# Optimization experiments

Measured on AMD Instinct MI355X. Metric: run time of the kernel, lower is better.

## Reference

```python
import jax, jax.numpy as jnp
import numpy as np

N = 16384          # number of units
K = 655
BOOST_STRENGTH = 1.0


def setup_inputs() -> dict:
    key = jax.random.key(0)
    k1, k2 = jax.random.split(key)
    x = jax.random.normal(k1, (4096, N), dtype=jnp.float32)
    dutyCycle = jax.random.uniform(k2, (N,), dtype=jnp.float32)
    return {"x": x, "dutyCycle": dutyCycle}


def reference(x, dutyCycle):
    # boost factor per unit: encourages under-used units
    targetDensity = K / x.shape[1]
    boostFactors = jnp.exp((targetDensity - dutyCycle) * BOOST_STRENGTH)  # (N,)
    boosted = x * boostFactors  # (B, N)
    # top-k per row, then scatter a binary mask of winners
    _, idx = jax.lax.top_k(boosted, K)  # (B, K)
    b = jnp.arange(x.shape[0])[:, None]  # (B, 1)
    res = jnp.zeros_like(x).at[b, idx].set(1.0)
    return res
```

## Files before the change

### kernel.cpp

```cpp
#include <hip/hip_runtime.h>
#include <math.h>
#include <stdint.h>


#define N_UNITS 16384
#define K_WIN 655
#define NT 512
#define NPROBE 11
#define SCAP 256
#define ITERS (N_UNITS / (NT * 4))

__device__ __forceinline__ uint32_t fkey(float f) {
    uint32_t b = __float_as_uint(f);
    uint32_t m = (uint32_t)((int32_t)b >> 31) | 0x80000000u;
    return b ^ m;
}

__global__ void boost_kernel(const float* __restrict__ duty,
                             float* __restrict__ bf, int n) {
    int i = blockIdx.x * blockDim.x + threadIdx.x;
    if (i < n) {
        const float td = 0.03997802734375f;
        float s = td - duty[i];
        bf[i] = (float)exp((double)s);
    }
}

__global__ __launch_bounds__(NT, 1) void kwinners_kernel(
    const float* __restrict__ x, const float* __restrict__ bf,
    float* __restrict__ out) {
    __shared__ uint32_t red[(NT / 64) * NPROBE];
    __shared__ int cglob[NPROBE];
    __shared__ uint32_t s_key[SCAP];
    __shared__ uint32_t s_idx[SCAP];
    __shared__ uint32_t bmap[N_UNITS / 32];
    __shared__ int sc[1];

    const int tid = threadIdx.x;
    const int lane = tid & 63;
    const int w = tid >> 6;
    const int row = blockIdx.x;
    const float4* xrow = (const float4*)(x + (size_t)row * N_UNITS);
    const float4* bfv = (const float4*)bf;
    float* orow = out + (size_t)row * N_UNITS;

    bmap[tid] = 0u;
    if (tid == 0) sc[0] = 0;

    uint32_t PF[NPROBE];
    {
        const float pv[NPROBE] = {1.90f, 1.70f, 1.55f, 1.43f, 1.33f, 1.25f,
                                  1.18f, 1.12f, 1.06f, 0.99f, 0.90f};
#pragma unroll
        for (int p = 0; p < NPROBE; ++p) PF[p] = fkey(pv[p]) | 0xFFFFu;
    }

    int cnt[NPROBE];
#pragma unroll
    for (int p = 0; p < NPROBE; ++p) cnt[p] = 0;

    uint4 kk[ITERS];

#pragma unroll
    for (int j = 0; j < ITERS; ++j) {
        int i4 = tid + j * NT;
        float4 xv = xrow[i4];
        float4 bv = bfv[i4];
        kk[j].x = fkey(xv.x * bv.x);
        kk[j].y = fkey(xv.y * bv.y);
        kk[j].z = fkey(xv.z * bv.z);
        kk[j].w = fkey(xv.w * bv.w);
#pragma unroll
        for (int p = 0; p < NPROBE; ++p)
            cnt[p] += (kk[j].x > PF[p]) + (kk[j].y > PF[p]) +
                      (kk[j].z > PF[p]) + (kk[j].w > PF[p]);
    }

    auto reduce_counts = [&]() {
#pragma unroll
        for (int p = 0; p < NPROBE; ++p) {
            int v = cnt[p];
#pragma unroll
            for (int m2 = 32; m2 >= 1; m2 >>= 1) v += __shfl_xor(v, m2, 64);
            if (lane == 0) red[w * NPROBE + p] = (uint32_t)v;
        }
        __syncthreads();
        if (tid < NPROBE) {
            int s = 0;
#pragma unroll
            for (int ww = 0; ww < NT / 64; ++ww) s += (int)red[ww * NPROBE + tid];
            cglob[tid] = s;
        }
        __syncthreads();
    };
    reduce_counts();

    long lo, hi;
    int cab, cgl;
    {
        int j = 0;
        while (j < NPROBE && cglob[j] < K_WIN) ++j;
        if (j == 0) {
            lo = (long)PF[0]; cgl = cglob[0]; hi = 0xFFFFFFFFL; cab = 0;
        } else if (j == NPROBE) {
            lo = -1; cgl = N_UNITS; hi = (long)PF[NPROBE - 1];
            cab = cglob[NPROBE - 1];
        } else {
            lo = (long)PF[j]; cgl = cglob[j]; hi = (long)PF[j - 1];
            cab = cglob[j - 1];
        }
    }
    int inB = cgl - cab;

    while (inB > SCAP && (hi - lo) > 1) {
        unsigned long range = (unsigned long)(hi - lo);
#pragma unroll
        for (int p = 0; p < NPROBE; ++p) {
            long Tp = lo + (long)(range * (unsigned long)(NPROBE - p) /
                                  (NPROBE + 1));
            int c = 0;
#pragma unroll
            for (int j = 0; j < ITERS; ++j)
                c += ((long)kk[j].x > Tp) + ((long)kk[j].y > Tp) +
                     ((long)kk[j].z > Tp) + ((long)kk[j].w > Tp);
            cnt[p] = c;
        }
        reduce_counts();
        int j = 0;
        while (j < NPROBE && cglob[j] < K_WIN) ++j;
        const long llo = lo;
        auto Tof = [&](int p) {
            return llo + (long)(range * (unsigned long)(NPROBE - p) /
                                (NPROBE + 1));
        };
        if (j == 0) {
            lo = Tof(0); cgl = cglob[0];
        } else if (j == NPROBE) {
            hi = Tof(NPROBE - 1); cab = cglob[NPROBE - 1];
        } else {
            lo = Tof(j); cgl = cglob[j]; hi = Tof(j - 1); cab = cglob[j - 1];
        }
        inB = cgl - cab;
    }
    const int need = K_WIN - cab;

    if (inB <= SCAP) {
#pragma unroll
        for (int j = 0; j < ITERS; ++j) {
            int base = (tid + j * NT) * 4;
            uint32_t kv[4] = {kk[j].x, kk[j].y, kk[j].z, kk[j].w};
#pragma unroll
            for (int e = 0; e < 4; ++e) {
                long k = (long)kv[e];
                if (k > lo && k <= hi) {
                    int p = atomicAdd(&sc[0], 1);
                    if (p < SCAP) {
                        s_key[p] = kv[e];
                        s_idx[p] = (uint32_t)(base + e);
                    }
                }
            }
        }
        __syncthreads();
        const int sS = sc[0];

        for (int jj = tid; jj < sS; jj += NT) {
            uint32_t myk = s_key[jj];
            uint32_t myi = s_idx[jj];
            int r = 0;
            for (int l = 0; l < sS; ++l) {
                uint32_t lk = s_key[l];
                r += (lk > myk) || (lk == myk && s_idx[l] < myi);
            }
            if (r < need) atomicOr(&bmap[myi >> 5], 1u << (myi & 31));
        }
    } else {
        if (tid == 0) {
            const float* xr = x + (size_t)row * N_UNITS;
            int r = 0;
            for (int i = 0; i < N_UNITS && r < need; ++i) {
                uint32_t kf = fkey(xr[i] * bf[i]);
                if ((long)kf == hi) {
                    bmap[i >> 5] |= (1u << (i & 31));
                    ++r;
                }
            }
        }
    }
    __syncthreads();

#pragma unroll
    for (int j = 0; j < ITERS; ++j) {
        int f = tid + j * NT;
        uint32_t bm = bmap[f >> 3];
        int sh = (f & 7) * 4;
        float4 o;
        o.x = (((long)kk[j].x > hi) || ((bm >> (sh + 0)) & 1u)) ? 1.0f : 0.0f;
        o.y = (((long)kk[j].y > hi) || ((bm >> (sh + 1)) & 1u)) ? 1.0f : 0.0f;
        o.z = (((long)kk[j].z > hi) || ((bm >> (sh + 2)) & 1u)) ? 1.0f : 0.0f;
        o.w = (((long)kk[j].w > hi) || ((bm >> (sh + 3)) & 1u)) ? 1.0f : 0.0f;
        ((float4*)orow)[f] = o;
    }
}

extern "C" void kernel_launch(void* const* d_in, const int* in_sizes, int n_in,
                              void* d_out, int out_size, void* d_ws,
                              size_t ws_size, hipStream_t stream) {
    const float* x = (const float*)d_in[0];
    const float* duty = (const float*)d_in[1];
    float* out = (float*)d_out;
    float* bf = (float*)d_ws;

    hipLaunchKernelGGL(boost_kernel, dim3(N_UNITS / 256), dim3(256), 0, stream,
                       duty, bf, N_UNITS);
    int rows = out_size / N_UNITS;
    hipLaunchKernelGGL(kwinners_kernel, dim3(rows), dim3(NT), 0, stream, x, bf,
                       out);
}
```

Baseline: 516.4 us.

## Prefetch row loads upfront, retune probe thresholds, pack keys for ranking

All x and boost-factor float4 loads for a row are issued before any key computation. This puts every load in flight at once and hides global-memory latency. The first-pass probe set drops from 11 to 7 thresholds concentrated near the expected cutoff, and the candidate buffer grows from 256 to 320, so fewer rows should need refinement passes. Candidate key and index are packed into one 64-bit value so ranking is a single compare, and the long compares become 32-bit compares. The cost is higher register pressure from holding the whole row twice.

New measurement: 439.0 us. 15.0% less time.

```diff
diff --git a/kernel.cpp b/kernel.cpp
--- a/kernel.cpp
+++ b/kernel.cpp
@@ -6,8 +6,8 @@
 #define N_UNITS 16384
 #define K_WIN 655
 #define NT 512
-#define NPROBE 11
-#define SCAP 256
+#define NPROBE 7
+#define SCAP 320
 #define ITERS (N_UNITS / (NT * 4))
 
 __device__ __forceinline__ uint32_t fkey(float f) {
@@ -31,8 +31,7 @@
     float* __restrict__ out) {
     __shared__ uint32_t red[(NT / 64) * NPROBE];
     __shared__ int cglob[NPROBE];
-    __shared__ uint32_t s_key[SCAP];
-    __shared__ uint32_t s_idx[SCAP];
+    __shared__ unsigned long long s_pk[SCAP];
     __shared__ uint32_t bmap[N_UNITS / 32];
     __shared__ int sc[1];
 
@@ -49,27 +48,30 @@
 
     uint32_t PF[NPROBE];
     {
-        const float pv[NPROBE] = {1.90f, 1.70f, 1.55f, 1.43f, 1.33f, 1.25f,
-                                  1.18f, 1.12f, 1.06f, 0.99f, 0.90f};
+        const float pv[NPROBE] = {1.45f, 1.32f, 1.24f, 1.20f,
+                                  1.16f, 1.10f, 1.00f};
 #pragma unroll
         for (int p = 0; p < NPROBE; ++p) PF[p] = fkey(pv[p]) | 0xFFFFu;
     }
 
+    float4 xv[ITERS];
+    float4 bv[ITERS];
+#pragma unroll
+    for (int j = 0; j < ITERS; ++j) xv[j] = xrow[tid + j * NT];
+#pragma unroll
+    for (int j = 0; j < ITERS; ++j) bv[j] = bfv[tid + j * NT];
+
     int cnt[NPROBE];
 #pragma unroll
     for (int p = 0; p < NPROBE; ++p) cnt[p] = 0;
 
     uint4 kk[ITERS];
-
 #pragma unroll
     for (int j = 0; j < ITERS; ++j) {
-        int i4 = tid + j * NT;
-        float4 xv = xrow[i4];
-        float4 bv = bfv[i4];
-        kk[j].x = fkey(xv.x * bv.x);
-        kk[j].y = fkey(xv.y * bv.y);
-        kk[j].z = fkey(xv.z * bv.z);
-        kk[j].w = fkey(xv.w * bv.w);
+        kk[j].x = fkey(xv[j].x * bv[j].x);
+        kk[j].y = fkey(xv[j].y * bv[j].y);
+        kk[j].z = fkey(xv[j].z * bv[j].z);
+        kk[j].w = fkey(xv[j].w * bv[j].w);
 #pragma unroll
         for (int p = 0; p < NPROBE; ++p)
             cnt[p] += (kk[j].x > PF[p]) + (kk[j].y > PF[p]) +
@@ -144,6 +146,10 @@
     }
     const int need = K_WIN - cab;
 
+    const uint32_t hi32 = (uint32_t)hi;
+    const uint32_t lo32 = (uint32_t)lo;
+    const bool lneg = (lo < 0);
+
     if (inB <= SCAP) {
 #pragma unroll
         for (int j = 0; j < ITERS; ++j) {
@@ -151,13 +157,12 @@
             uint32_t kv[4] = {kk[j].x, kk[j].y, kk[j].z, kk[j].w};
 #pragma unroll
             for (int e = 0; e < 4; ++e) {
-                long k = (long)kv[e];
-                if (k > lo && k <= hi) {
+                bool in = ((kv[e] > lo32) || lneg) && (kv[e] <= hi32);
+                if (in) {
                     int p = atomicAdd(&sc[0], 1);
-                    if (p < SCAP) {
-                        s_key[p] = kv[e];
-                        s_idx[p] = (uint32_t)(base + e);
-                    }
+                    if (p < SCAP)
+                        s_pk[p] = ((unsigned long long)kv[e] << 32) |
+                                  (uint32_t)(~(uint32_t)(base + e));
                 }
             }
         }
@@ -165,14 +170,13 @@
         const int sS = sc[0];
 
         for (int jj = tid; jj < sS; jj += NT) {
-            uint32_t myk = s_key[jj];
-            uint32_t myi = s_idx[jj];
+            unsigned long long my = s_pk[jj];
             int r = 0;
-            for (int l = 0; l < sS; ++l) {
-                uint32_t lk = s_key[l];
-                r += (lk > myk) || (lk == myk && s_idx[l] < myi);
+            for (int l = 0; l < sS; ++l) r += (s_pk[l] > my);
+            if (r < need) {
+                uint32_t myi = ~(uint32_t)my;
+                atomicOr(&bmap[myi >> 5], 1u << (myi & 31));
             }
-            if (r < need) atomicOr(&bmap[myi >> 5], 1u << (myi & 31));
         }
     } else {
         if (tid == 0) {
@@ -195,10 +199,10 @@
         uint32_t bm = bmap[f >> 3];
         int sh = (f & 7) * 4;
         float4 o;
-        o.x = (((long)kk[j].x > hi) || ((bm >> (sh + 0)) & 1u)) ? 1.0f : 0.0f;
-        o.y = (((long)kk[j].y > hi) || ((bm >> (sh + 1)) & 1u)) ? 1.0f : 0.0f;
-        o.z = (((long)kk[j].z > hi) || ((bm >> (sh + 2)) & 1u)) ? 1.0f : 0.0f;
-        o.w = (((long)kk[j].w > hi) || ((bm >> (sh + 3)) & 1u)) ? 1.0f : 0.0f;
+        o.x = ((kk[j].x > hi32) || ((bm >> (sh + 0)) & 1u)) ? 1.0f : 0.0f;
+        o.y = ((kk[j].y > hi32) || ((bm >> (sh + 1)) & 1u)) ? 1.0f : 0.0f;
+        o.z = ((kk[j].z > hi32) || ((bm >> (sh + 2)) & 1u)) ? 1.0f : 0.0f;
+        o.w = ((kk[j].w > hi32) || ((bm >> (sh + 3)) & 1u)) ? 1.0f : 0.0f;
         ((float4*)orow)[f] = o;
     }
 }
```
